# Kernel tuning notes

Measured on AMD Instinct MI355X. Metric: run time of the kernel, lower is better.

The kernel has to match this reference:

```python
import jax, jax.numpy as jnp
import numpy as np

N_NODES = 100000
N_EDGES = 3200000
IN_CH = 256
OUT_CH = 128


def setup_inputs() -> dict:
    key = jax.random.key(0)
    k1, k2, k3, k4, k5 = jax.random.split(key, 5)
    x = jax.random.normal(k1, (N_NODES, IN_CH), dtype=jnp.float32)
    # xavier_uniform init for the linear weight (stored as [in, out])
    limit = float(np.sqrt(6.0 / (IN_CH + OUT_CH)))
    W = jax.random.uniform(k2, (IN_CH, OUT_CH), dtype=jnp.float32,
                           minval=-limit, maxval=limit)
    b = jnp.zeros((OUT_CH,), dtype=jnp.float32)  # init.zeros_
    edge_row = jax.random.randint(k3, (N_EDGES,), 0, N_NODES, dtype=jnp.int32)
    edge_col = jax.random.randint(k4, (N_EDGES,), 0, N_NODES, dtype=jnp.int32)
    edge_val = jax.random.uniform(k5, (N_EDGES,), dtype=jnp.float32)
    return {"x": x, "W": W, "b": b,
            "edge_row": edge_row, "edge_col": edge_col, "edge_val": edge_val}


def reference(x, W, b, edge_row, edge_col, edge_val):
    # x = self.lin(x)
    h = x @ W + b  # [N, out]
    # out = torch.sparse.mm(adj_norm, h): out[r] = sum_e val[e] * h[col[e]] for row[e]==r
    msgs = edge_val[:, None] * h[edge_col]  # [E, out] gather + scale
    out = jax.ops.segment_sum(msgs, edge_row, num_segments=N_NODES)  # scatter-add
    return out
```

## Files before the change

kernel.cpp:

```cpp
#include <hip/hip_runtime.h>
#include <hip/hip_bf16.h>

#define N_NODES 100000
#define N_EDGES 3200000
#define IN_CH   256
#define OUT_CH  128

#define RPB 64
#define NBUCKET 1563
#define NBLK 256
#define PART_T 1024
#define SS_T 1024
#define CHUNK (N_EDGES / NBLK)
#define CHUNK4 (CHUNK / 4)
#define CAP 2816
#define AGG_T 512
#define QREG 6

typedef int   iv4 __attribute__((ext_vector_type(4)));
typedef float fv4 __attribute__((ext_vector_type(4)));
typedef short bf16x8 __attribute__((ext_vector_type(8)));
typedef float f32x4 __attribute__((ext_vector_type(4)));
typedef unsigned long long u64;
typedef unsigned short ushort_t;

__device__ __forceinline__ unsigned bfr(float f) {
  unsigned u = __float_as_uint(f);
  return (u + 0x7FFFu + ((u >> 16) & 1u)) >> 16;
}

__global__ __launch_bounds__(256) void wt_prep_kernel(
    const float* __restrict__ W, ushort_t* __restrict__ wt) {
  const int T = blockIdx.x * 256 + threadIdx.x;
  const int col = T >> 6;
  const int k0 = (T & 63) * 4;
  uint2 pk;
  pk.x = bfr(W[(size_t)(k0 + 0) * OUT_CH + col]) |
         (bfr(W[(size_t)(k0 + 1) * OUT_CH + col]) << 16);
  pk.y = bfr(W[(size_t)(k0 + 2) * OUT_CH + col]) |
         (bfr(W[(size_t)(k0 + 3) * OUT_CH + col]) << 16);
  *reinterpret_cast<uint2*>(wt + (size_t)col * IN_CH + k0) = pk;
}

#define GR 32

__global__ __launch_bounds__(256) void gemm_mfma_kernel(
    const float* __restrict__ x, const ushort_t* __restrict__ wt,
    const float* __restrict__ b, ushort_t* __restrict__ hb) {
  __shared__ alignas(16) char xs[GR * 512];
  __shared__ alignas(16) char ws[128 * 512];

  const int tid = threadIdx.x;
  const int row0 = blockIdx.x * GR;

#pragma unroll
  for (int it = 0; it < 8; ++it) {
    int f = it * 256 + tid;
    int r = f >> 6, k4 = f & 63;
    fv4 v = *reinterpret_cast<const fv4*>(x + (size_t)(row0 + r) * IN_CH + k4 * 4);
    uint2 pk;
    pk.x = bfr(v.x) | (bfr(v.y) << 16);
    pk.y = bfr(v.z) | (bfr(v.w) << 16);
    unsigned off = (unsigned)(r * 512) + (((unsigned)(k4 * 8)) ^ ((unsigned)(r & 7) << 4));
    *reinterpret_cast<uint2*>(xs + off) = pk;
  }
#pragma unroll
  for (int it = 0; it < 16; ++it) {
    int f = it * 256 + tid;
    int col = f >> 5, ch = f & 31;
    bf16x8 v = *reinterpret_cast<const bf16x8*>(wt + (size_t)col * IN_CH + ch * 8);
    unsigned off = (unsigned)(col * 512) + (((unsigned)(ch * 16)) ^ ((unsigned)(col & 7) << 4));
    *reinterpret_cast<bf16x8*>(ws + off) = v;
  }
  __syncthreads();

  const int w = tid >> 6, l = tid & 63;
  const int lr = l & 15, lk = l >> 4;
  const int arow = (w & 1) * 16 + lr;
  const int cb = (w >> 1) * 64;

  f32x4 acc[4];
#pragma unroll
  for (int n = 0; n < 4; ++n) {
    int c0 = cb + n * 16 + lk * 4;
    acc[n] = (f32x4){b[c0], b[c0 + 1], b[c0 + 2], b[c0 + 3]};
  }

  const unsigned axm = (unsigned)(arow & 7) << 4;
#pragma unroll
  for (int kk = 0; kk < 8; ++kk) {
    bf16x8 af = *reinterpret_cast<const bf16x8*>(
        xs + (unsigned)(arow * 512) + (((unsigned)(kk * 64 + lk * 16)) ^ axm));
#pragma unroll
    for (int n = 0; n < 4; ++n) {
      int bcol = cb + n * 16 + lr;
      bf16x8 bf_ = *reinterpret_cast<const bf16x8*>(
          ws + (unsigned)(bcol * 512) +
          (((unsigned)(kk * 64 + lk * 16)) ^ ((unsigned)(bcol & 7) << 4)));
      acc[n] = __builtin_amdgcn_mfma_f32_16x16x32_bf16(bf_, af, acc[n], 0, 0, 0);
    }
  }

  const int grow = row0 + arow;
#pragma unroll
  for (int n = 0; n < 4; ++n) {
    int c0 = cb + n * 16 + lk * 4;
    uint2 pk;
    pk.x = bfr(acc[n][0]) | (bfr(acc[n][1]) << 16);
    pk.y = bfr(acc[n][2]) | (bfr(acc[n][3]) << 16);
    *reinterpret_cast<uint2*>(hb + (size_t)grow * OUT_CH + c0) = pk;
  }
}

__global__ __launch_bounds__(PART_T) void histA_kernel(
    const int* __restrict__ erow, int* __restrict__ histA) {
  __shared__ int hcnt[NBUCKET];
  const int blk = blockIdx.x, tid = threadIdx.x;
  for (int i = tid; i < NBUCKET; i += PART_T) hcnt[i] = 0;
  __syncthreads();
  const iv4* er4 = reinterpret_cast<const iv4*>(erow) + blk * CHUNK4;
  for (int i = tid; i < CHUNK4; i += PART_T) {
    iv4 r4 = __builtin_nontemporal_load(er4 + i);
    atomicAdd(&hcnt[r4.x >> 6], 1);
    atomicAdd(&hcnt[r4.y >> 6], 1);
    atomicAdd(&hcnt[r4.z >> 6], 1);
    atomicAdd(&hcnt[r4.w >> 6], 1);
  }
  __syncthreads();
  for (int b2 = tid; b2 < NBUCKET; b2 += PART_T)
    histA[b2 * NBLK + blk] = hcnt[b2];
}

__global__ __launch_bounds__(256) void scanA_partial(
    const int* __restrict__ a, int* __restrict__ bsum) {
  __shared__ int s[256];
  const int t = threadIdx.x;
  s[t] = a[blockIdx.x * 256 + t];
  __syncthreads();
#pragma unroll
  for (int d = 128; d > 0; d >>= 1) {
    if (t < d) s[t] += s[t + d];
    __syncthreads();
  }
  if (t == 0) bsum[blockIdx.x] = s[0];
}

__global__ __launch_bounds__(1024) void scanA_bsums(int* __restrict__ bsum) {
  __shared__ int s[1024];
  const int t = threadIdx.x;
  const int i0 = 2 * t, i1 = 2 * t + 1;
  const int v0 = (i0 < NBUCKET) ? bsum[i0] : 0;
  const int v1 = (i1 < NBUCKET) ? bsum[i1] : 0;
  s[t] = v0 + v1;
  __syncthreads();
  for (int d = 1; d < 1024; d <<= 1) {
    int u = (t >= d) ? s[t - d] : 0;
    __syncthreads();
    s[t] += u;
    __syncthreads();
  }
  const int ex = (t == 0) ? 0 : s[t - 1];
  if (i0 < NBUCKET) bsum[i0] = ex;
  if (i1 < NBUCKET) bsum[i1] = ex + v0;
}

__global__ __launch_bounds__(256) void scanA_apply(
    int* __restrict__ a, const int* __restrict__ bsum) {
  __shared__ int s[256];
  const int t = threadIdx.x;
  const int idx = blockIdx.x * 256 + t;
  const int v = a[idx];
  s[t] = v;
  __syncthreads();
  for (int d = 1; d < 256; d <<= 1) {
    int u = (t >= d) ? s[t - d] : 0;
    __syncthreads();
    s[t] += u;
    __syncthreads();
  }
  a[idx] = s[t] - v + bsum[blockIdx.x];
}

__global__ __launch_bounds__(SS_T) void sortscatter_kernel(
    const int* __restrict__ erow, const int* __restrict__ ecol,
    const float* __restrict__ eval, const int* __restrict__ scanA,
    u64* __restrict__ tmp) {
  __shared__ u64 sorted_q[CHUNK];
  __shared__ ushort_t bkt[CHUNK];
  __shared__ int cursor[NBUCKET];
  __shared__ int delta[NBUCKET];

  const int blk = blockIdx.x, tid = threadIdx.x;
  int* sarr = reinterpret_cast<int*>(sorted_q);

  const int b0 = 2 * tid, b1 = 2 * tid + 1;
  int c0 = 0, c1 = 0, g0 = 0, g1 = 0;
  if (b0 < NBUCKET) {
    int idx = b0 * NBLK + blk;
    g0 = scanA[idx];
    int nxt = (idx + 1 < NBUCKET * NBLK) ? scanA[idx + 1] : N_EDGES;
    c0 = nxt - g0;
  }
  if (b1 < NBUCKET) {
    int idx = b1 * NBLK + blk;
    g1 = scanA[idx];
    int nxt = (idx + 1 < NBUCKET * NBLK) ? scanA[idx + 1] : N_EDGES;
    c1 = nxt - g1;
  }
  sarr[tid] = c0 + c1;
  __syncthreads();
  for (int d = 1; d < SS_T; d <<= 1) {
    int v = (tid >= d) ? sarr[tid - d] : 0;
    __syncthreads();
    sarr[tid] += v;
    __syncthreads();
  }
  const int pref = (tid == 0) ? 0 : sarr[tid - 1];
  __syncthreads();
  if (b0 < NBUCKET) { cursor[b0] = pref;      delta[b0] = g0 - pref; }
  if (b1 < NBUCKET) { cursor[b1] = pref + c0; delta[b1] = g1 - (pref + c0); }
  __syncthreads();

  const iv4* er4 = reinterpret_cast<const iv4*>(erow) + blk * CHUNK4;
  const iv4* ec4 = reinterpret_cast<const iv4*>(ecol) + blk * CHUNK4;
  const fv4* ev4 = reinterpret_cast<const fv4*>(eval) + blk * CHUNK4;
  for (int i = tid; i < CHUNK4; i += SS_T) {
    iv4 r4 = __builtin_nontemporal_load(er4 + i);
    iv4 c4 = __builtin_nontemporal_load(ec4 + i);
    fv4 v4 = __builtin_nontemporal_load(ev4 + i);
#pragma unroll
    for (int j = 0; j < 4; ++j) {
      int r = r4[j];
      int bb = r >> 6;
      int pos = atomicAdd(&cursor[bb], 1);
      sorted_q[pos] = ((u64)(unsigned)__float_as_int(v4[j]) << 32) |
                      ((unsigned)(r & 63) << 17) | (unsigned)c4[j];
      bkt[pos] = (ushort_t)bb;
    }
  }
  __syncthreads();

  for (int i = tid; i < CHUNK; i += SS_T) {
    u64 q = sorted_q[i];
    int dst = i + delta[bkt[i]];
    __builtin_nontemporal_store(q, tmp + dst);
  }
}

__global__ __launch_bounds__(AGG_T) void bucket_agg_kernel(
    const ushort_t* __restrict__ hb, const u64* __restrict__ tmp,
    const int* __restrict__ scanA, float* __restrict__ out) {
  __shared__ u64 eds[CAP];
  __shared__ int rcnt[RPB];
  __shared__ int rstart[RPB + 1];
  __shared__ int rcur[RPB];
  __shared__ int sscan[RPB];

  const int bkt = blockIdx.x, tid = threadIdx.x;
  const int base = scanA[bkt * NBLK];
  const int end = (bkt == NBUCKET - 1) ? N_EDGES : scanA[(bkt + 1) * NBLK];
  const int cnt = end - base;
  const int row0 = bkt * RPB;
  const unsigned* __restrict__ h32 = reinterpret_cast<const unsigned*>(hb);
  const int w = tid >> 6, lane = tid & 63;

  if (cnt <= CAP) {
    if (tid < RPB) rcnt[tid] = 0;
    __syncthreads();

    u64 qreg[QREG];
#pragma unroll
    for (int j = 0; j < QREG; ++j) {
      int i = j * AGG_T + tid;
      if (i < cnt) {
        qreg[j] = __builtin_nontemporal_load(tmp + base + i);
        atomicAdd(&rcnt[(unsigned)(qreg[j] >> 17) & 63u], 1);
      }
    }
    __syncthreads();

    if (tid < RPB) sscan[tid] = rcnt[tid];
    __syncthreads();
    for (int d = 1; d < RPB; d <<= 1) {
      int v = (tid < RPB && tid >= d) ? sscan[tid - d] : 0;
      __syncthreads();
      if (tid < RPB) sscan[tid] += v;
      __syncthreads();
    }
    if (tid < RPB) rstart[tid + 1] = sscan[tid];
    if (tid == 0) rstart[0] = 0;
    __syncthreads();
    if (tid < RPB) rcur[tid] = rstart[tid];
    __syncthreads();

#pragma unroll
    for (int j = 0; j < QREG; ++j) {
      int i = j * AGG_T + tid;
      if (i < cnt) {
        u64 q = qreg[j];
        int r = (unsigned)(q >> 17) & 63u;
        int pos = atomicAdd(&rcur[r], 1);
        eds[pos] = q;
      }
    }
    __syncthreads();

    for (int r = w; r < RPB; r += AGG_T / 64) {
      int grow = row0 + r;
      if (grow >= N_NODES) break;
      int e = rstart[r], e2 = rstart[r + 1];
      float ax = 0.f, ay = 0.f;
      for (; e + 3 < e2; e += 4) {
        u64 q0 = eds[e + 0], q1 = eds[e + 1];
        u64 q2 = eds[e + 2], q3 = eds[e + 3];
        unsigned u0 = h32[(size_t)(unsigned)(q0 & 0x1FFFFu) * 64 + lane];
        unsigned u1 = h32[(size_t)(unsigned)(q1 & 0x1FFFFu) * 64 + lane];
        unsigned u2 = h32[(size_t)(unsigned)(q2 & 0x1FFFFu) * 64 + lane];
        unsigned u3 = h32[(size_t)(unsigned)(q3 & 0x1FFFFu) * 64 + lane];
        float v0 = __int_as_float((int)(q0 >> 32));
        float v1 = __int_as_float((int)(q1 >> 32));
        float v2 = __int_as_float((int)(q2 >> 32));
        float v3 = __int_as_float((int)(q3 >> 32));
        ax += v0 * __uint_as_float(u0 << 16) + v1 * __uint_as_float(u1 << 16) +
              v2 * __uint_as_float(u2 << 16) + v3 * __uint_as_float(u3 << 16);
        ay += v0 * __uint_as_float(u0 & 0xFFFF0000u) +
              v1 * __uint_as_float(u1 & 0xFFFF0000u) +
              v2 * __uint_as_float(u2 & 0xFFFF0000u) +
              v3 * __uint_as_float(u3 & 0xFFFF0000u);
      }
      for (; e < e2; ++e) {
        u64 q = eds[e];
        unsigned u = h32[(size_t)(unsigned)(q & 0x1FFFFu) * 64 + lane];
        float v = __int_as_float((int)(q >> 32));
        ax += v * __uint_as_float(u << 16);
        ay += v * __uint_as_float(u & 0xFFFF0000u);
      }
      reinterpret_cast<float2*>(out)[(size_t)grow * 64 + lane] =
          make_float2(ax, ay);
    }
  } else {
    for (int i = tid; i < RPB * 64; i += AGG_T) {
      int grow = row0 + (i >> 6);
      if (grow < N_NODES)
        reinterpret_cast<float2*>(out)[(size_t)grow * 64 + (i & 63)] =
            make_float2(0.f, 0.f);
    }
    __syncthreads();
    for (int i = w; i < cnt; i += AGG_T / 64) {
      u64 q = tmp[base + i];
      int r = (unsigned)(q >> 17) & 63u;
      unsigned col = (unsigned)(q & 0x1FFFFu);
      float v = __int_as_float((int)(q >> 32));
      unsigned u = h32[(size_t)col * 64 + lane];
      if (row0 + r < N_NODES) {
        atomicAdd(out + (size_t)(row0 + r) * OUT_CH + lane * 2,
                  v * __uint_as_float(u << 16));
        atomicAdd(out + (size_t)(row0 + r) * OUT_CH + lane * 2 + 1,
                  v * __uint_as_float(u & 0xFFFF0000u));
      }
    }
  }
}

extern "C" void kernel_launch(void* const* d_in, const int* in_sizes, int n_in,
                              void* d_out, int out_size, void* d_ws,
                              size_t ws_size, hipStream_t stream) {
  const float* x    = (const float*)d_in[0];
  const float* W    = (const float*)d_in[1];
  const float* b    = (const float*)d_in[2];
  const int* erow   = (const int*)d_in[3];
  const int* ecol   = (const int*)d_in[4];
  const float* eval = (const float*)d_in[5];
  float* out = (float*)d_out;

  char* wsb = (char*)d_ws;
  ushort_t* hb  = (ushort_t*)(wsb);
  u64* tmp      = (u64*)(wsb + 25600000);
  int* scanA    = (int*)(wsb + 51200000);
  int* bsum     = (int*)(wsb + 52800512);
  ushort_t* wt  = (ushort_t*)(wsb + 52806764 + 4);

  wt_prep_kernel<<<32, 256, 0, stream>>>(W, wt);
  gemm_mfma_kernel<<<N_NODES / GR, 256, 0, stream>>>(x, wt, b, hb);

  histA_kernel<<<NBLK, PART_T, 0, stream>>>(erow, scanA);
  scanA_partial<<<NBUCKET, 256, 0, stream>>>(scanA, bsum);
  scanA_bsums<<<1, 1024, 0, stream>>>(bsum);
  scanA_apply<<<NBUCKET, 256, 0, stream>>>(scanA, bsum);
  sortscatter_kernel<<<NBLK, SS_T, 0, stream>>>(erow, ecol, eval, scanA, tmp);

  bucket_agg_kernel<<<NBUCKET, AGG_T, 0, stream>>>(hb, tmp, scanA, out);
}
```

Before: 199.9 us.

## Sort bucket edges by column slice so waves gather h rows in cache-friendly order

In the aggregation kernel, edges inside each 64-row bucket are now counted-sorted by a composite key: a column slice taken from bits 13-16 of the column index, plus the row. Each wave owns 8 rows and walks all 13 slices in order, keeping 8 accumulator pairs in registers. The aim is for all waves to touch a similar region of h at roughly the same time, which should improve L2/MALL hit rates on the random gathers. The cost is a larger 1024-entry histogram and scan, more registers, and a shorter inner unroll (2 instead of 4), which lowers memory-level parallelism per wave.

```diff
diff --git a/kernel.cpp b/kernel.cpp
--- a/kernel.cpp
+++ b/kernel.cpp
@@ -16,6 +16,9 @@
 #define CAP 2816
 #define AGG_T 512
 #define QREG 6
+#define NSLICE 13
+#define NKEY (NSLICE * 64)
+#define NKEYP 1024
 
 typedef int   iv4 __attribute__((ext_vector_type(4)));
 typedef float fv4 __attribute__((ext_vector_type(4)));
@@ -251,10 +254,10 @@
     const ushort_t* __restrict__ hb, const u64* __restrict__ tmp,
     const int* __restrict__ scanA, float* __restrict__ out) {
   __shared__ u64 eds[CAP];
-  __shared__ int rcnt[RPB];
-  __shared__ int rstart[RPB + 1];
-  __shared__ int rcur[RPB];
-  __shared__ int sscan[RPB];
+  __shared__ int rcnt[NKEYP];
+  __shared__ int rstart[NKEYP];
+  __shared__ int rcur[NKEY];
+  __shared__ int s512[AGG_T];
 
   const int bkt = blockIdx.x, tid = threadIdx.x;
   const int base = scanA[bkt * NBLK];
@@ -265,7 +268,8 @@
   const int w = tid >> 6, lane = tid & 63;
 
   if (cnt <= CAP) {
-    if (tid < RPB) rcnt[tid] = 0;
+    rcnt[tid] = 0;
+    rcnt[tid + AGG_T] = 0;
     __syncthreads();
 
     u64 qreg[QREG];
@@ -273,24 +277,28 @@
     for (int j = 0; j < QREG; ++j) {
       int i = j * AGG_T + tid;
       if (i < cnt) {
-        qreg[j] = __builtin_nontemporal_load(tmp + base + i);
-        atomicAdd(&rcnt[(unsigned)(qreg[j] >> 17) & 63u], 1);
+        u64 q = __builtin_nontemporal_load(tmp + base + i);
+        qreg[j] = q;
+        int key = (int)(((q >> 13) & 0x0Fu) << 6) | (int)((q >> 17) & 63u);
+        atomicAdd(&rcnt[key], 1);
       }
     }
     __syncthreads();
 
-    if (tid < RPB) sscan[tid] = rcnt[tid];
-    __syncthreads();
-    for (int d = 1; d < RPB; d <<= 1) {
-      int v = (tid < RPB && tid >= d) ? sscan[tid - d] : 0;
+    const int v0 = rcnt[2 * tid], v1 = rcnt[2 * tid + 1];
+    s512[tid] = v0 + v1;
+    __syncthreads();
+    for (int d = 1; d < AGG_T; d <<= 1) {
+      int u = (tid >= d) ? s512[tid - d] : 0;
       __syncthreads();
-      if (tid < RPB) sscan[tid] += v;
+      s512[tid] += u;
       __syncthreads();
     }
-    if (tid < RPB) rstart[tid + 1] = sscan[tid];
-    if (tid == 0) rstart[0] = 0;
-    __syncthreads();
-    if (tid < RPB) rcur[tid] = rstart[tid];
+    const int ex = (tid == 0) ? 0 : s512[tid - 1];
+    rstart[2 * tid] = ex;
+    rstart[2 * tid + 1] = ex + v0;
+    if (2 * tid < NKEY) rcur[2 * tid] = ex;
+    if (2 * tid + 1 < NKEY) rcur[2 * tid + 1] = ex + v0;
     __syncthreads();
 
 #pragma unroll
@@ -298,45 +306,51 @@
       int i = j * AGG_T + tid;
       if (i < cnt) {
         u64 q = qreg[j];
-        int r = (unsigned)(q >> 17) & 63u;
-        int pos = atomicAdd(&rcur[r], 1);
+        int key = (int)(((q >> 13) & 0x0Fu) << 6) | (int)((q >> 17) & 63u);
+        int pos = atomicAdd(&rcur[key], 1);
         eds[pos] = q;
       }
     }
     __syncthreads();
 
-    for (int r = w; r < RPB; r += AGG_T / 64) {
-      int grow = row0 + r;
-      if (grow >= N_NODES) break;
-      int e = rstart[r], e2 = rstart[r + 1];
-      float ax = 0.f, ay = 0.f;
-      for (; e + 3 < e2; e += 4) {
-        u64 q0 = eds[e + 0], q1 = eds[e + 1];
-        u64 q2 = eds[e + 2], q3 = eds[e + 3];
-        unsigned u0 = h32[(size_t)(unsigned)(q0 & 0x1FFFFu) * 64 + lane];
-        unsigned u1 = h32[(size_t)(unsigned)(q1 & 0x1FFFFu) * 64 + lane];
-        unsigned u2 = h32[(size_t)(unsigned)(q2 & 0x1FFFFu) * 64 + lane];
-        unsigned u3 = h32[(size_t)(unsigned)(q3 & 0x1FFFFu) * 64 + lane];
-        float v0 = __int_as_float((int)(q0 >> 32));
-        float v1 = __int_as_float((int)(q1 >> 32));
-        float v2 = __int_as_float((int)(q2 >> 32));
-        float v3 = __int_as_float((int)(q3 >> 32));
-        ax += v0 * __uint_as_float(u0 << 16) + v1 * __uint_as_float(u1 << 16) +
-              v2 * __uint_as_float(u2 << 16) + v3 * __uint_as_float(u3 << 16);
-        ay += v0 * __uint_as_float(u0 & 0xFFFF0000u) +
-              v1 * __uint_as_float(u1 & 0xFFFF0000u) +
-              v2 * __uint_as_float(u2 & 0xFFFF0000u) +
-              v3 * __uint_as_float(u3 & 0xFFFF0000u);
+    const int r0 = w * 8;
+    float ax[8], ay[8];
+#pragma unroll
+    for (int ri = 0; ri < 8; ++ri) { ax[ri] = 0.f; ay[ri] = 0.f; }
+
+    for (int s = 0; s < NSLICE; ++s) {
+#pragma unroll
+      for (int ri = 0; ri < 8; ++ri) {
+        const int key = (s << 6) | (r0 + ri);
+        int e = rstart[key];
+        const int e2 = rstart[key + 1];
+        for (; e + 1 < e2; e += 2) {
+          u64 q0 = eds[e], q1 = eds[e + 1];
+          unsigned u0 = h32[(size_t)(unsigned)(q0 & 0x1FFFFu) * 64 + lane];
+          unsigned u1 = h32[(size_t)(unsigned)(q1 & 0x1FFFFu) * 64 + lane];
+          float v0 = __int_as_float((int)(q0 >> 32));
+          float v1 = __int_as_float((int)(q1 >> 32));
+          ax[ri] += v0 * __uint_as_float(u0 << 16) +
+                    v1 * __uint_as_float(u1 << 16);
+          ay[ri] += v0 * __uint_as_float(u0 & 0xFFFF0000u) +
+                    v1 * __uint_as_float(u1 & 0xFFFF0000u);
+        }
+        if (e < e2) {
+          u64 q = eds[e];
+          unsigned u = h32[(size_t)(unsigned)(q & 0x1FFFFu) * 64 + lane];
+          float v = __int_as_float((int)(q >> 32));
+          ax[ri] += v * __uint_as_float(u << 16);
+          ay[ri] += v * __uint_as_float(u & 0xFFFF0000u);
+        }
       }
-      for (; e < e2; ++e) {
-        u64 q = eds[e];
-        unsigned u = h32[(size_t)(unsigned)(q & 0x1FFFFu) * 64 + lane];
-        float v = __int_as_float((int)(q >> 32));
-        ax += v * __uint_as_float(u << 16);
-        ay += v * __uint_as_float(u & 0xFFFF0000u);
-      }
-      reinterpret_cast<float2*>(out)[(size_t)grow * 64 + lane] =
-          make_float2(ax, ay);
+    }
+
+#pragma unroll
+    for (int ri = 0; ri < 8; ++ri) {
+      const int grow = row0 + r0 + ri;
+      if (grow < N_NODES)
+        reinterpret_cast<float2*>(out)[(size_t)grow * 64 + lane] =
+            make_float2(ax[ri], ay[ri]);
     }
   } else {
     for (int i = tid; i < RPB * 64; i += AGG_T) {
```

Result: slower. 231.6 us (+15.9%).

## Fuse row histogram into GEMM launch and unroll aggregation gather by eight

Applied to the files above, without the earlier changes.

The histogram pass over edge rows now runs as extra blocks inside the GEMM kernel launch, so the independent histogram and GEMM work overlap and one kernel launch is removed. Histogram blocks now use 256 threads instead of 1024, and every block of the combined kernel allocates the full 80KB shared buffer. Separately, the aggregation inner loop is unrolled from 4 to 8 edges, issuing all gathers before accumulating to raise memory-level parallelism at the cost of more registers.

```diff
diff --git a/kernel.cpp b/kernel.cpp
--- a/kernel.cpp
+++ b/kernel.cpp
@@ -9,13 +9,14 @@
 #define RPB 64
 #define NBUCKET 1563
 #define NBLK 256
-#define PART_T 1024
 #define SS_T 1024
 #define CHUNK (N_EDGES / NBLK)
 #define CHUNK4 (CHUNK / 4)
 #define CAP 2816
 #define AGG_T 512
 #define QREG 6
+#define GR 32
+#define GEMM_BLKS (N_NODES / GR)
 
 typedef int   iv4 __attribute__((ext_vector_type(4)));
 typedef float fv4 __attribute__((ext_vector_type(4)));
@@ -42,16 +43,36 @@
   *reinterpret_cast<uint2*>(wt + (size_t)col * IN_CH + k0) = pk;
 }
 
-#define GR 32
-
-__global__ __launch_bounds__(256) void gemm_mfma_kernel(
+__global__ __launch_bounds__(256) void gemm_hist_kernel(
     const float* __restrict__ x, const ushort_t* __restrict__ wt,
-    const float* __restrict__ b, ushort_t* __restrict__ hb) {
-  __shared__ alignas(16) char xs[GR * 512];
-  __shared__ alignas(16) char ws[128 * 512];
+    const float* __restrict__ b, ushort_t* __restrict__ hb,
+    const int* __restrict__ erow, int* __restrict__ histA) {
+  __shared__ alignas(16) char smem[81920];
 
   const int tid = threadIdx.x;
-  const int row0 = blockIdx.x * GR;
+
+  if (blockIdx.x < NBLK) {
+    int* hcnt = reinterpret_cast<int*>(smem);
+    const int blk = blockIdx.x;
+    for (int i = tid; i < NBUCKET; i += 256) hcnt[i] = 0;
+    __syncthreads();
+    const iv4* er4 = reinterpret_cast<const iv4*>(erow) + blk * CHUNK4;
+    for (int i = tid; i < CHUNK4; i += 256) {
+      iv4 r4 = __builtin_nontemporal_load(er4 + i);
+      atomicAdd(&hcnt[r4.x >> 6], 1);
+      atomicAdd(&hcnt[r4.y >> 6], 1);
+      atomicAdd(&hcnt[r4.z >> 6], 1);
+      atomicAdd(&hcnt[r4.w >> 6], 1);
+    }
+    __syncthreads();
+    for (int b2 = tid; b2 < NBUCKET; b2 += 256)
+      histA[b2 * NBLK + blk] = hcnt[b2];
+    return;
+  }
+
+  char* xs = smem;
+  char* ws = smem + 16384;
+  const int row0 = (blockIdx.x - NBLK) * GR;
 
 #pragma unroll
   for (int it = 0; it < 8; ++it) {
@@ -112,25 +133,6 @@
   }
 }
 
-__global__ __launch_bounds__(PART_T) void histA_kernel(
-    const int* __restrict__ erow, int* __restrict__ histA) {
-  __shared__ int hcnt[NBUCKET];
-  const int blk = blockIdx.x, tid = threadIdx.x;
-  for (int i = tid; i < NBUCKET; i += PART_T) hcnt[i] = 0;
-  __syncthreads();
-  const iv4* er4 = reinterpret_cast<const iv4*>(erow) + blk * CHUNK4;
-  for (int i = tid; i < CHUNK4; i += PART_T) {
-    iv4 r4 = __builtin_nontemporal_load(er4 + i);
-    atomicAdd(&hcnt[r4.x >> 6], 1);
-    atomicAdd(&hcnt[r4.y >> 6], 1);
-    atomicAdd(&hcnt[r4.z >> 6], 1);
-    atomicAdd(&hcnt[r4.w >> 6], 1);
-  }
-  __syncthreads();
-  for (int b2 = tid; b2 < NBUCKET; b2 += PART_T)
-    histA[b2 * NBLK + blk] = hcnt[b2];
-}
-
 __global__ __launch_bounds__(256) void scanA_partial(
     const int* __restrict__ a, int* __restrict__ bsum) {
   __shared__ int s[256];
@@ -310,23 +312,20 @@
       if (grow >= N_NODES) break;
       int e = rstart[r], e2 = rstart[r + 1];
       float ax = 0.f, ay = 0.f;
-      for (; e + 3 < e2; e += 4) {
-        u64 q0 = eds[e + 0], q1 = eds[e + 1];
-        u64 q2 = eds[e + 2], q3 = eds[e + 3];
-        unsigned u0 = h32[(size_t)(unsigned)(q0 & 0x1FFFFu) * 64 + lane];
-        unsigned u1 = h32[(size_t)(unsigned)(q1 & 0x1FFFFu) * 64 + lane];
-        unsigned u2 = h32[(size_t)(unsigned)(q2 & 0x1FFFFu) * 64 + lane];
-        unsigned u3 = h32[(size_t)(unsigned)(q3 & 0x1FFFFu) * 64 + lane];
-        float v0 = __int_as_float((int)(q0 >> 32));
-        float v1 = __int_as_float((int)(q1 >> 32));
-        float v2 = __int_as_float((int)(q2 >> 32));
-        float v3 = __int_as_float((int)(q3 >> 32));
-        ax += v0 * __uint_as_float(u0 << 16) + v1 * __uint_as_float(u1 << 16) +
-              v2 * __uint_as_float(u2 << 16) + v3 * __uint_as_float(u3 << 16);
-        ay += v0 * __uint_as_float(u0 & 0xFFFF0000u) +
-              v1 * __uint_as_float(u1 & 0xFFFF0000u) +
-              v2 * __uint_as_float(u2 & 0xFFFF0000u) +
-              v3 * __uint_as_float(u3 & 0xFFFF0000u);
+      for (; e + 7 < e2; e += 8) {
+        u64 q[8];
+#pragma unroll
+        for (int j = 0; j < 8; ++j) q[j] = eds[e + j];
+        unsigned g[8];
+#pragma unroll
+        for (int j = 0; j < 8; ++j)
+          g[j] = h32[(size_t)(unsigned)(q[j] & 0x1FFFFu) * 64 + lane];
+#pragma unroll
+        for (int j = 0; j < 8; ++j) {
+          float v = __int_as_float((int)(q[j] >> 32));
+          ax += v * __uint_as_float(g[j] << 16);
+          ay += v * __uint_as_float(g[j] & 0xFFFF0000u);
+        }
       }
       for (; e < e2; ++e) {
         u64 q = eds[e];
@@ -381,9 +380,10 @@
   ushort_t* wt  = (ushort_t*)(wsb + 52806764 + 4);
 
   wt_prep_kernel<<<32, 256, 0, stream>>>(W, wt);
-  gemm_mfma_kernel<<<N_NODES / GR, 256, 0, stream>>>(x, wt, b, hb);
-
-  histA_kernel<<<NBLK, PART_T, 0, stream>>>(erow, scanA);
+
+  gemm_hist_kernel<<<NBLK + GEMM_BLKS, 256, 0, stream>>>(x, wt, b, hb, erow,
+                                                         scanA);
+
   scanA_partial<<<NBUCKET, 256, 0, stream>>>(scanA, bsum);
   scanA_bsums<<<1, 1024, 0, stream>>>(bsum);
   scanA_apply<<<NBUCKET, 256, 0, stream>>>(scanA, bsum);
```

Result: no change. 198.8 us (-0.5%).
